# Kernel optimization log

Measured on AMD Instinct MI355X. Metric: run time of the kernel, lower is better.

Reference implementation:

```python
import jax, jax.numpy as jnp
import numpy as np

N = 50000      # nodes
E = 800000     # edges
IN = 128       # in_channels
HID = 32       # hidden_channels per head
HEADS = 4
OUT = 16       # out_channels
NEG_SLOPE_ATT = 0.2   # GATv2Conv default negative_slope
NEG_SLOPE_ACT = 0.01  # F.leaky_relu default
EPS = 1e-16


def setup_inputs() -> dict:
    key = jax.random.key(0)
    ks = jax.random.split(key, 13)
    d1 = HEADS * HID  # 128
    g = lambda k, shape, fan: jax.random.normal(k, shape, jnp.float32) * (1.0 / np.sqrt(fan))
    return {
        "x": jax.random.normal(ks[0], (N, IN), jnp.float32),
        "edge_index": jax.random.randint(ks[1], (2, E), 0, N, dtype=jnp.int32),
        "edge_weight": jax.random.uniform(ks[2], (E,), jnp.float32),
        # conv1 (GATv2): lin_l, lin_r, att, bias
        "Wl1": g(ks[3], (IN, d1), IN), "Wr1": g(ks[4], (IN, d1), IN),
        "att1": g(ks[5], (HEADS, HID), HID), "b1": jnp.zeros((d1,), jnp.float32),
        # conv2
        "Wl2": g(ks[6], (d1, d1), d1), "Wr2": g(ks[7], (d1, d1), d1),
        "att2": g(ks[8], (HEADS, HID), HID), "b2": jnp.zeros((d1,), jnp.float32),
        # classifier
        "Wc": g(ks[9], (d1, OUT), d1), "bc": jnp.zeros((OUT,), jnp.float32),
    }


def gatv2_layer(x, Wl, Wr, att, bias, src, dst):
    n = x.shape[0]
    xl = (x @ Wl).reshape(n, HEADS, HID)  # source transform
    xr = (x @ Wr).reshape(n, HEADS, HID)  # target transform
    m = xl[src] + xr[dst]                                    # [Etot, H, C]
    e = jnp.sum(jax.nn.leaky_relu(m, NEG_SLOPE_ATT) * att, axis=-1)  # [Etot, H]
    # segment softmax over incoming edges of each target node
    emax = jax.ops.segment_max(e, dst, num_segments=n)       # [N, H]
    ex = jnp.exp(e - emax[dst])
    denom = jax.ops.segment_sum(ex, dst, num_segments=n)     # [N, H]
    alpha = ex / (denom[dst] + EPS)                          # [Etot, H]
    out = jax.ops.segment_sum(xl[src] * alpha[:, :, None], dst, num_segments=n)  # [N, H, C]
    return out.reshape(n, HEADS * HID) + bias


def reference(x, edge_index, edge_weight, Wl1, Wr1, att1, b1, Wl2, Wr2, att2, b2, Wc, bc):
    # GATv2Conv default add_self_loops=True
    loops = jnp.arange(N, dtype=edge_index.dtype)
    src = jnp.concatenate([edge_index[0], loops])
    dst = jnp.concatenate([edge_index[1], loops])
    h = gatv2_layer(x, Wl1, Wr1, att1, b1, src, dst)
    h = jax.nn.leaky_relu(h, NEG_SLOPE_ACT)
    h = gatv2_layer(h, Wl2, Wr2, att2, b2, src, dst)
    h = jax.nn.leaky_relu(h, NEG_SLOPE_ACT)
    logits = h @ Wc + bc
    return (logits, h)
```

## Files before the change

### kernel.cpp

```cpp
#include <hip/hip_runtime.h>
#include <hip/hip_fp16.h>


#define LOG2E 1.4426950408889634f
#define AST 40

typedef short bf16x8 __attribute__((ext_vector_type(8)));
typedef float f32x4 __attribute__((ext_vector_type(4)));

__device__ __forceinline__ unsigned short f2bf(float f) {
  union { float f; unsigned u; } x; x.f = f;
  unsigned r = x.u + 0x7fffu + ((x.u >> 16) & 1u);
  return (unsigned short)(r >> 16);
}
__device__ __forceinline__ float bf2f(unsigned short h) {
  union { unsigned u; float f; } x; x.u = ((unsigned)h) << 16;
  return x.f;
}
__device__ __forceinline__ void split4(float4 v, ushort4& h, ushort4& l) {
  h.x = f2bf(v.x); l.x = f2bf(v.x - bf2f(h.x));
  h.y = f2bf(v.y); l.y = f2bf(v.y - bf2f(h.y));
  h.z = f2bf(v.z); l.z = f2bf(v.z - bf2f(h.z));
  h.w = f2bf(v.w); l.w = f2bf(v.w - bf2f(h.w));
}


__global__ __launch_bounds__(256) void zero_i32(int* __restrict__ p, int n) {
  int i = blockIdx.x * 256 + threadIdx.x;
  if (i < n) p[i] = 0;
}

__global__ __launch_bounds__(256) void count_kernel(const int* __restrict__ dst,
                                                    int* __restrict__ cnt, int E) {
  int i = blockIdx.x * 256 + threadIdx.x;
  if (i < E) atomicAdd(&cnt[dst[i]], 1);
}

__global__ __launch_bounds__(256) void scan_blk(const int* __restrict__ cnt,
                                                int* __restrict__ excl,
                                                int* __restrict__ bsum, int n) {
  __shared__ int s[256];
  int t = threadIdx.x, i = blockIdx.x * 256 + t;
  int v = (i < n) ? (cnt[i] + 1) : 0;
  s[t] = v;
  __syncthreads();
#pragma unroll
  for (int off = 1; off < 256; off <<= 1) {
    int u = (t >= off) ? s[t - off] : 0;
    __syncthreads();
    s[t] += u;
    __syncthreads();
  }
  if (i < n) excl[i] = s[t] - v;
  if (t == 255) bsum[blockIdx.x] = s[255];
}

__global__ __launch_bounds__(256) void scan_bsum(int* __restrict__ bsum, int nb,
                                                 int* __restrict__ row_start, int n) {
  __shared__ int s[256];
  int t = threadIdx.x;
  int v = (t < nb) ? bsum[t] : 0;
  s[t] = v;
  __syncthreads();
#pragma unroll
  for (int off = 1; off < 256; off <<= 1) {
    int u = (t >= off) ? s[t - off] : 0;
    __syncthreads();
    s[t] += u;
    __syncthreads();
  }
  if (t < nb) bsum[t] = s[t] - v;
  if (t == 255) row_start[n] = s[255];
}

__global__ __launch_bounds__(256) void scan_add(int* __restrict__ row_start,
                                                const int* __restrict__ bsum,
                                                int* __restrict__ wpos,
                                                int* __restrict__ csr,
                                                int n, int padBase) {
  int i = blockIdx.x * 256 + threadIdx.x;
  if (i < n) {
    int r = row_start[i] + bsum[blockIdx.x];
    row_start[i] = r;
    wpos[i] = r + 1;
    csr[r] = i;
  }
  if (blockIdx.x == 0 && threadIdx.x < 16) csr[padBase + threadIdx.x] = 0;
}

__global__ __launch_bounds__(256) void scatter_kernel(const int* __restrict__ src,
                                                      const int* __restrict__ dst,
                                                      int* __restrict__ wpos,
                                                      int* __restrict__ csr,
                                                      int E, int sliceSize) {
  int slice = blockIdx.x & 7;
  int chunk = blockIdx.x >> 3;
  int nchunk = gridDim.x >> 3;
  int lo = slice * sliceSize, hi = lo + sliceSize;
  int per = (E + nchunk - 1) / nchunk;
  int b = chunk * per;
  int e = min(b + per, E);
  for (int i = b + threadIdx.x; i < e; i += 256) {
    int d = dst[i];
    if (d >= lo && d < hi) {
      int p = atomicAdd(&wpos[d], 1);
      csr[p] = src[i];
    }
  }
}

__global__ __launch_bounds__(256) void convert_W(const float* __restrict__ Wl1,
                                                 const float* __restrict__ Wr1,
                                                 const float* __restrict__ Wl2,
                                                 const float* __restrict__ Wr2,
                                                 unsigned short* __restrict__ BT1h,
                                                 unsigned short* __restrict__ BT1l,
                                                 unsigned short* __restrict__ BT2h,
                                                 unsigned short* __restrict__ BT2l) {
  int b = blockIdx.x;
  const float* Wl = (b < 128) ? Wl1 : Wl2;
  const float* Wr = (b < 128) ? Wr1 : Wr2;
  unsigned short* BTh = (b < 128) ? BT1h : BT2h;
  unsigned short* BTl = (b < 128) ? BT1l : BT2l;
  int idx = (b & 127) * 256 + threadIdx.x;
  int col = idx >> 7, k = idx & 127;
  float v = (col < 128) ? Wl[k * 128 + col] : Wr[k * 128 + (col - 128)];
  unsigned short h = f2bf(v);
  BTh[idx] = h;
  BTl[idx] = f2bf(v - bf2f(h));
}

enum { IN_F32 = 0, IN_F16 = 1 };
template <int MODE>
__global__ __launch_bounds__(256) void gemm_mfma(
    const float* __restrict__ Af, const __half* __restrict__ Af16,
    const unsigned short* __restrict__ BTh, const unsigned short* __restrict__ BTl,
    __half* __restrict__ Cl, __half* __restrict__ Cr, int nrows) {
  __shared__ unsigned short sAh[128 * AST], sAl[128 * AST];
  __shared__ unsigned short sBh[128 * AST], sBl[128 * AST];
  int tid = threadIdx.x;
  int wave = tid >> 6, lane = tid & 63;
  int rowBase = blockIdx.x * 128;
  int colBase = blockIdx.y * 128;
  int rowHalf = (wave >> 1) * 64;
  int colHalf = (wave & 1) * 64;
  int l15 = lane & 15, quad = lane >> 4;

  f32x4 acc[4][4];
#pragma unroll
  for (int m = 0; m < 4; ++m)
#pragma unroll
    for (int n = 0; n < 4; ++n) acc[m][n] = (f32x4){0.f, 0.f, 0.f, 0.f};

  for (int kc = 0; kc < 4; ++kc) {
#pragma unroll
    for (int i = 0; i < 2; ++i) {
      int idx = tid + i * 256;
      int row = idx >> 2, seg = idx & 3;
      int gr = rowBase + row;
      if (MODE == IN_F32) {
        float4 v0 = make_float4(0.f, 0.f, 0.f, 0.f), v1 = v0;
        if (gr < nrows) {
          v0 = *(const float4*)&Af[(size_t)gr * 128 + kc * 32 + seg * 8];
          v1 = *(const float4*)&Af[(size_t)gr * 128 + kc * 32 + seg * 8 + 4];
        }
        ushort4 h0, l0, h1, l1;
        split4(v0, h0, l0);
        split4(v1, h1, l1);
        *(ushort4*)&sAh[row * AST + seg * 8] = h0;
        *(ushort4*)&sAh[row * AST + seg * 8 + 4] = h1;
        *(ushort4*)&sAl[row * AST + seg * 8] = l0;
        *(ushort4*)&sAl[row * AST + seg * 8 + 4] = l1;
      } else {
        uint4 raw = make_uint4(0, 0, 0, 0);
        if (gr < nrows)
          raw = *(const uint4*)&Af16[(size_t)gr * 128 + kc * 32 + seg * 8];
        const __half* hp = (const __half*)&raw;
        float4 v0 = make_float4(__half2float(hp[0]), __half2float(hp[1]),
                                __half2float(hp[2]), __half2float(hp[3]));
        float4 v1 = make_float4(__half2float(hp[4]), __half2float(hp[5]),
                                __half2float(hp[6]), __half2float(hp[7]));
        ushort4 h0, l0, h1, l1;
        split4(v0, h0, l0);
        split4(v1, h1, l1);
        *(ushort4*)&sAh[row * AST + seg * 8] = h0;
        *(ushort4*)&sAh[row * AST + seg * 8 + 4] = h1;
        *(ushort4*)&sAl[row * AST + seg * 8] = l0;
        *(ushort4*)&sAl[row * AST + seg * 8 + 4] = l1;
      }
    }
#pragma unroll
    for (int i = 0; i < 2; ++i) {
      int idx = tid + i * 256;
      int col = idx >> 2, seg = idx & 3;
      *(uint4*)&sBh[col * AST + seg * 8] =
          *(const uint4*)&BTh[(size_t)(colBase + col) * 128 + kc * 32 + seg * 8];
      *(uint4*)&sBl[col * AST + seg * 8] =
          *(const uint4*)&BTl[(size_t)(colBase + col) * 128 + kc * 32 + seg * 8];
    }
    __syncthreads();

    bf16x8 afh[4], afl[4], bfh[4], bfl[4];
#pragma unroll
    for (int m = 0; m < 4; ++m) {
      int r = rowHalf + m * 16 + l15;
      afh[m] = *(const bf16x8*)&sAh[r * AST + quad * 8];
      afl[m] = *(const bf16x8*)&sAl[r * AST + quad * 8];
    }
#pragma unroll
    for (int n = 0; n < 4; ++n) {
      int cc = colHalf + n * 16 + l15;
      bfh[n] = *(const bf16x8*)&sBh[cc * AST + quad * 8];
      bfl[n] = *(const bf16x8*)&sBl[cc * AST + quad * 8];
    }
#pragma unroll
    for (int m = 0; m < 4; ++m)
#pragma unroll
      for (int n = 0; n < 4; ++n) {
        acc[m][n] = __builtin_amdgcn_mfma_f32_16x16x32_bf16(afh[m], bfh[n], acc[m][n], 0, 0, 0);
        acc[m][n] = __builtin_amdgcn_mfma_f32_16x16x32_bf16(afh[m], bfl[n], acc[m][n], 0, 0, 0);
        acc[m][n] = __builtin_amdgcn_mfma_f32_16x16x32_bf16(afl[m], bfh[n], acc[m][n], 0, 0, 0);
      }
    __syncthreads();
  }

  __half* __restrict__ C = (blockIdx.y == 0) ? Cl : Cr;
#pragma unroll
  for (int m = 0; m < 4; ++m)
#pragma unroll
    for (int r = 0; r < 4; ++r) {
      int grow = rowBase + rowHalf + m * 16 + quad * 4 + r;
      if (grow < nrows) {
#pragma unroll
        for (int n = 0; n < 4; ++n)
          C[(size_t)grow * 128 + colHalf + n * 16 + l15] = __float2half(acc[m][n][r]);
      }
    }
}

__global__ __launch_bounds__(256) void gat_attn(const __half* __restrict__ xl,
                                                const __half* __restrict__ xr,
                                                const int* __restrict__ row_start,
                                                const int* __restrict__ csr,
                                                const float* __restrict__ att,
                                                const float* __restrict__ bias,
                                                float* __restrict__ ofp,
                                                __half* __restrict__ oh16,
                                                int n_nodes) {
  int node = blockIdx.x * 4 + (threadIdx.x >> 6);
  if (node >= n_nodes) return;
  int lane = threadIdx.x & 63;
  int slot = lane >> 4;
  int l15 = lane & 15;
  int c0 = l15 * 8;

  float fxr[8];
  {
    uint4 raw = *(const uint4*)&xr[(size_t)node * 128 + c0];
    const __half* hp = (const __half*)&raw;
#pragma unroll
    for (int k = 0; k < 8; ++k) fxr[k] = __half2float(hp[k]);
  }
  float a06[8], a04[8];
  {
    float4 a0 = *(const float4*)&att[c0];
    float4 a1 = *(const float4*)&att[c0 + 4];
    float av[8] = {a0.x, a0.y, a0.z, a0.w, a1.x, a1.y, a1.z, a1.w};
    const float C06 = 0.6f * LOG2E, C04 = 0.4f * LOG2E;
#pragma unroll
    for (int k = 0; k < 8; ++k) { a06[k] = av[k] * C06; a04[k] = av[k] * C04; }
  }

  float acc[8];
#pragma unroll
  for (int k = 0; k < 8; ++k) acc[k] = 0.f;
  float lsum = 0.f;

#define EDGE_BODY(SRC, PVALID)                                                 \
  {                                                                            \
    uint4 raw = *(const uint4*)&xl[(size_t)(unsigned)(SRC)*128 + c0];          \
    const __half* hp = (const __half*)&raw;                                    \
    float e = 0.f;                                                             \
    _Pragma("unroll") for (int k = 0; k < 8; ++k) {                            \
      float t = __half2float(hp[k]) + fxr[k];                                  \
      e = fmaf(a06[k], t, e);                                                  \
      e = fmaf(a04[k], fabsf(t), e);                                           \
    }                                                                          \
    e += __shfl_xor(e, 1);                                                     \
    e += __shfl_xor(e, 2);                                                     \
    float p = (PVALID) ? __builtin_amdgcn_exp2f(e) : 0.f;                      \
    lsum += p;                                                                 \
    _Pragma("unroll") for (int k = 0; k < 8; ++k)                              \
        acc[k] = fmaf(p, __half2float(hp[k]), acc[k]);                         \
  }

  int beg = row_start[node], end = row_start[node + 1];
  int deg = end - beg;
  int fullEnd = beg + (deg & ~15);

  for (int base = beg; base < fullEnd; base += 16) {
    int b0 = base + 4 * slot;
    int s0 = csr[b0], s1 = csr[b0 + 1], s2 = csr[b0 + 2], s3 = csr[b0 + 3];
    EDGE_BODY(s0, true);
    EDGE_BODY(s1, true);
    EDGE_BODY(s2, true);
    EDGE_BODY(s3, true);
  }
  for (int base = fullEnd; base < end; base += 4) {
    int idx = base + slot;
    int src = csr[idx];
    EDGE_BODY(src, idx < end);
  }
#undef EDGE_BODY

  lsum += __shfl_xor(lsum, 16);
  lsum += __shfl_xor(lsum, 32);
#pragma unroll
  for (int k = 0; k < 8; ++k) {
    acc[k] += __shfl_xor(acc[k], 16);
    acc[k] += __shfl_xor(acc[k], 32);
  }

  if (slot == 0) {
    float4 b0v = *(const float4*)&bias[c0];
    float4 b1v = *(const float4*)&bias[c0 + 4];
    float bv[8] = {b0v.x, b0v.y, b0v.z, b0v.w, b1v.x, b1v.y, b1v.z, b1v.w};
    float inv = 1.f / (lsum + 1e-16f);
    float o[8];
#pragma unroll
    for (int k = 0; k < 8; ++k) {
      float v = fmaf(acc[k], inv, bv[k]);
      o[k] = fmaf(0.495f, fabsf(v), 0.505f * v);
    }
    if (ofp) {
      *(float4*)&ofp[(size_t)node * 128 + c0] = make_float4(o[0], o[1], o[2], o[3]);
      *(float4*)&ofp[(size_t)node * 128 + c0 + 4] = make_float4(o[4], o[5], o[6], o[7]);
    }
    if (oh16) {
      ushort4 ha, hb;
      ha.x = __half_as_ushort(__float2half(o[0]));
      ha.y = __half_as_ushort(__float2half(o[1]));
      ha.z = __half_as_ushort(__float2half(o[2]));
      ha.w = __half_as_ushort(__float2half(o[3]));
      hb.x = __half_as_ushort(__float2half(o[4]));
      hb.y = __half_as_ushort(__float2half(o[5]));
      hb.z = __half_as_ushort(__float2half(o[6]));
      hb.w = __half_as_ushort(__float2half(o[7]));
      *(ushort4*)&oh16[(size_t)node * 128 + c0] = ha;
      *(ushort4*)&oh16[(size_t)node * 128 + c0 + 4] = hb;
    }
  }
}

__global__ __launch_bounds__(256) void classifier_kernel(const float4* __restrict__ h4,
                                                         const float* __restrict__ Wc,
                                                         const float* __restrict__ bc,
                                                         float* __restrict__ logits,
                                                         int n) {
  __shared__ float sW[2048];
  __shared__ float sb[16];
  int t = threadIdx.x;
#pragma unroll
  for (int i = 0; i < 8; ++i) sW[t + i * 256] = Wc[t + i * 256];
  if (t < 16) sb[t] = bc[t];
  __syncthreads();
  int node = blockIdx.x * 256 + t;
  if (node >= n) return;
  float acc[16];
#pragma unroll
  for (int o = 0; o < 16; ++o) acc[o] = sb[o];
  for (int c4 = 0; c4 < 32; ++c4) {
    float4 hv = h4[(unsigned)node * 32 + c4];
    const float* w = &sW[c4 * 64];
#pragma unroll
    for (int o = 0; o < 16; ++o) {
      acc[o] = fmaf(hv.x, w[o], acc[o]);
      acc[o] = fmaf(hv.y, w[16 + o], acc[o]);
      acc[o] = fmaf(hv.z, w[32 + o], acc[o]);
      acc[o] = fmaf(hv.w, w[48 + o], acc[o]);
    }
  }
#pragma unroll
  for (int q = 0; q < 4; ++q)
    *(float4*)&logits[(size_t)node * 16 + q * 4] =
        make_float4(acc[q * 4], acc[q * 4 + 1], acc[q * 4 + 2], acc[q * 4 + 3]);
}


extern "C" void kernel_launch(void* const* d_in, const int* in_sizes, int n_in,
                              void* d_out, int out_size, void* d_ws, size_t ws_size,
                              hipStream_t stream) {
  const float* x    = (const float*)d_in[0];
  const int*   ei   = (const int*)d_in[1];
  const float* Wl1  = (const float*)d_in[3];
  const float* Wr1  = (const float*)d_in[4];
  const float* att1 = (const float*)d_in[5];
  const float* b1   = (const float*)d_in[6];
  const float* Wl2  = (const float*)d_in[7];
  const float* Wr2  = (const float*)d_in[8];
  const float* att2 = (const float*)d_in[9];
  const float* b2   = (const float*)d_in[10];
  const float* Wc   = (const float*)d_in[11];
  const float* bc   = (const float*)d_in[12];

  const int N = in_sizes[0] / 128;
  const int E = in_sizes[1] / 2;

  float* outp   = (float*)d_out;
  float* logits = outp;
  float* hout   = outp + (size_t)N * 16;
  __half* h1f16 = (__half*)hout;

  char* ws = (char*)d_ws;
  __half* xlbuf = (__half*)ws;                ws += (size_t)N * 128 * 2;
  __half* xrbuf = (__half*)ws;                ws += (size_t)N * 128 * 2;
  unsigned short* WT1h = (unsigned short*)ws; ws += 256 * 128 * 2;
  unsigned short* WT1l = (unsigned short*)ws; ws += 256 * 128 * 2;
  unsigned short* WT2h = (unsigned short*)ws; ws += 256 * 128 * 2;
  unsigned short* WT2l = (unsigned short*)ws; ws += 256 * 128 * 2;
  int* cnt       = (int*)ws;                  ws += (size_t)N * 4;
  int* row_start = (int*)ws;                  ws += (size_t)(N + 1) * 4;
  int* wpos      = (int*)ws;                  ws += (size_t)N * 4;
  int* bsum      = (int*)ws;                  ws += 256 * 4;
  int* csr       = (int*)ws;                  ws += (size_t)(E + N + 16) * 4;

  const int* esrc = ei;
  const int* edst = ei + E;

  int gN = (N + 255) / 256, gE = (E + 255) / 256;
  dim3 gGemm((N + 127) / 128, 2);
  int gAttn = (N + 3) / 4;
  int sliceSize = (N + 7) / 8;

  zero_i32<<<gN, 256, 0, stream>>>(cnt, N);
  count_kernel<<<gE, 256, 0, stream>>>(edst, cnt, E);
  scan_blk<<<gN, 256, 0, stream>>>(cnt, row_start, bsum, N);
  scan_bsum<<<1, 256, 0, stream>>>(bsum, gN, row_start, N);
  scan_add<<<gN, 256, 0, stream>>>(row_start, bsum, wpos, csr, N, E + N);
  scatter_kernel<<<1024, 256, 0, stream>>>(esrc, edst, wpos, csr, E, sliceSize);

  convert_W<<<256, 256, 0, stream>>>(Wl1, Wr1, Wl2, Wr2, WT1h, WT1l, WT2h, WT2l);

  gemm_mfma<IN_F32><<<gGemm, 256, 0, stream>>>(x, nullptr, WT1h, WT1l,
                                               xlbuf, xrbuf, N);
  gat_attn<<<gAttn, 256, 0, stream>>>(xlbuf, xrbuf, row_start, csr, att1, b1,
                                      nullptr, h1f16, N);

  gemm_mfma<IN_F16><<<gGemm, 256, 0, stream>>>(nullptr, h1f16, WT2h, WT2l,
                                               xlbuf, xrbuf, N);
  gat_attn<<<gAttn, 256, 0, stream>>>(xlbuf, xrbuf, row_start, csr, att2, b2,
                                      hout, nullptr, N);

  classifier_kernel<<<(N + 255) / 256, 256, 0, stream>>>((const float4*)hout, Wc, bc,
                                                         logits, N);
}
```

Measured before the change: 323.3 us.

## Fuse CSR scatter into layer-1 GEMM, merge count with weight conversion, use packed fp16 math

```diff
diff --git a/kernel.cpp b/kernel.cpp
--- a/kernel.cpp
+++ b/kernel.cpp
@@ -24,16 +24,41 @@
   h.w = f2bf(v.w); l.w = f2bf(v.w - bf2f(h.w));
 }
 
+__device__ __forceinline__ float mixlo(float a, unsigned b, float c) {
+  float d;
+  asm("v_fma_mix_f32 %0, %1, %2, %3 op_sel_hi:[0,1,0]"
+      : "=v"(d) : "v"(a), "v"(b), "v"(c));
+  return d;
+}
+__device__ __forceinline__ float mixhi(float a, unsigned b, float c) {
+  float d;
+  asm("v_fma_mix_f32 %0, %1, %2, %3 op_sel:[0,1,0] op_sel_hi:[0,1,0]"
+      : "=v"(d) : "v"(a), "v"(b), "v"(c));
+  return d;
+}
+__device__ __forceinline__ float mixlo_abs(float a, unsigned b, float c) {
+  float d;
+  asm("v_fma_mix_f32 %0, %1, |%2|, %3 op_sel_hi:[0,1,0]"
+      : "=v"(d) : "v"(a), "v"(b), "v"(c));
+  return d;
+}
+__device__ __forceinline__ float mixhi_abs(float a, unsigned b, float c) {
+  float d;
+  asm("v_fma_mix_f32 %0, %1, |%2|, %3 op_sel:[0,1,0] op_sel_hi:[0,1,0]"
+      : "=v"(d) : "v"(a), "v"(b), "v"(c));
+  return d;
+}
+__device__ __forceinline__ unsigned pk_add(unsigned a, unsigned b) {
+  union { unsigned u; __half2 h; } x, y, r;
+  x.u = a; y.u = b;
+  r.h = __hadd2(x.h, y.h);
+  return r.u;
+}
+
 
 __global__ __launch_bounds__(256) void zero_i32(int* __restrict__ p, int n) {
   int i = blockIdx.x * 256 + threadIdx.x;
   if (i < n) p[i] = 0;
-}
-
-__global__ __launch_bounds__(256) void count_kernel(const int* __restrict__ dst,
-                                                    int* __restrict__ cnt, int E) {
-  int i = blockIdx.x * 256 + threadIdx.x;
-  if (i < E) atomicAdd(&cnt[dst[i]], 1);
 }
 
 __global__ __launch_bounds__(256) void scan_blk(const int* __restrict__ cnt,
@@ -88,36 +113,18 @@
   if (blockIdx.x == 0 && threadIdx.x < 16) csr[padBase + threadIdx.x] = 0;
 }
 
-__global__ __launch_bounds__(256) void scatter_kernel(const int* __restrict__ src,
-                                                      const int* __restrict__ dst,
-                                                      int* __restrict__ wpos,
-                                                      int* __restrict__ csr,
-                                                      int E, int sliceSize) {
-  int slice = blockIdx.x & 7;
-  int chunk = blockIdx.x >> 3;
-  int nchunk = gridDim.x >> 3;
-  int lo = slice * sliceSize, hi = lo + sliceSize;
-  int per = (E + nchunk - 1) / nchunk;
-  int b = chunk * per;
-  int e = min(b + per, E);
-  for (int i = b + threadIdx.x; i < e; i += 256) {
-    int d = dst[i];
-    if (d >= lo && d < hi) {
-      int p = atomicAdd(&wpos[d], 1);
-      csr[p] = src[i];
-    }
-  }
-}
-
-__global__ __launch_bounds__(256) void convert_W(const float* __restrict__ Wl1,
-                                                 const float* __restrict__ Wr1,
-                                                 const float* __restrict__ Wl2,
-                                                 const float* __restrict__ Wr2,
-                                                 unsigned short* __restrict__ BT1h,
-                                                 unsigned short* __restrict__ BT1l,
-                                                 unsigned short* __restrict__ BT2h,
-                                                 unsigned short* __restrict__ BT2l) {
+__global__ __launch_bounds__(256) void convert_count(
+    const float* __restrict__ Wl1, const float* __restrict__ Wr1,
+    const float* __restrict__ Wl2, const float* __restrict__ Wr2,
+    unsigned short* __restrict__ BT1h, unsigned short* __restrict__ BT1l,
+    unsigned short* __restrict__ BT2h, unsigned short* __restrict__ BT2l,
+    const int* __restrict__ dst, int* __restrict__ cnt, int E) {
   int b = blockIdx.x;
+  if (b >= 256) {
+    int i = (b - 256) * 256 + threadIdx.x;
+    if (i < E) atomicAdd(&cnt[dst[i]], 1);
+    return;
+  }
   const float* Wl = (b < 128) ? Wl1 : Wl2;
   const float* Wr = (b < 128) ? Wr1 : Wr2;
   unsigned short* BTh = (b < 128) ? BT1h : BT2h;
@@ -130,18 +137,66 @@
   BTl[idx] = f2bf(v - bf2f(h));
 }
 
-enum { IN_F32 = 0, IN_F16 = 1 };
-template <int MODE>
+enum { IN_F32 = 0, IN_BFPAIR = 1 };
+template <int MODE, int FUSE>
 __global__ __launch_bounds__(256) void gemm_mfma(
-    const float* __restrict__ Af, const __half* __restrict__ Af16,
+    const float* __restrict__ Af,
+    const unsigned short* __restrict__ Ah, const unsigned short* __restrict__ Al,
     const unsigned short* __restrict__ BTh, const unsigned short* __restrict__ BTl,
-    __half* __restrict__ Cl, __half* __restrict__ Cr, int nrows) {
-  __shared__ unsigned short sAh[128 * AST], sAl[128 * AST];
-  __shared__ unsigned short sBh[128 * AST], sBl[128 * AST];
+    __half* __restrict__ Cl, __half* __restrict__ Cr, int nrows,
+    const int* __restrict__ esrc, const int* __restrict__ edst,
+    int* __restrict__ wpos, int* __restrict__ csr, int E, int sliceSize) {
+  __shared__ __align__(16) unsigned short smem[4 * 128 * AST];
   int tid = threadIdx.x;
+  int bx, by;
+  if (FUSE) {
+    int g = blockIdx.x / 9, r = blockIdx.x - g * 9;
+    if (r < 5) {
+      int sid = g * 5 + r;
+      if (sid < 1024) {
+        int per = (E + 1023) >> 10;
+        int b0 = sid * per;
+        int cnt = min(per, E - b0);
+        if (cnt > 0) {
+          int* ss = (int*)smem;
+          int* sd = ss + per;
+          for (int i = tid; i < cnt; i += 256) {
+            ss[i] = esrc[b0 + i];
+            sd[i] = edst[b0 + i];
+          }
+          __syncthreads();
+          for (int sl = 0; sl < 8; ++sl) {
+            int lo = sl * sliceSize, hi = lo + sliceSize;
+            for (int i = tid; i < cnt; i += 256) {
+              int d = sd[i];
+              if (d >= lo && d < hi) {
+                int p = atomicAdd(&wpos[d], 1);
+                csr[p] = ss[i];
+              }
+            }
+          }
+        }
+      }
+      return;
+    }
+    int gid = g * 4 + (r - 5);
+    int nbx = (nrows + 127) >> 7;
+    if (gid >= nbx * 2) return;
+    bx = gid >> 1;
+    by = gid & 1;
+  } else {
+    bx = blockIdx.x;
+    by = blockIdx.y;
+  }
+
+  unsigned short* sAh = smem;
+  unsigned short* sAl = smem + 5120;
+  unsigned short* sBh = smem + 10240;
+  unsigned short* sBl = smem + 15360;
+
   int wave = tid >> 6, lane = tid & 63;
-  int rowBase = blockIdx.x * 128;
-  int colBase = blockIdx.y * 128;
+  int rowBase = bx * 128;
+  int colBase = by * 128;
   int rowHalf = (wave >> 1) * 64;
   int colHalf = (wave & 1) * 64;
   int l15 = lane & 15, quad = lane >> 4;
@@ -172,21 +227,13 @@
         *(ushort4*)&sAl[row * AST + seg * 8] = l0;
         *(ushort4*)&sAl[row * AST + seg * 8 + 4] = l1;
       } else {
-        uint4 raw = make_uint4(0, 0, 0, 0);
-        if (gr < nrows)
-          raw = *(const uint4*)&Af16[(size_t)gr * 128 + kc * 32 + seg * 8];
-        const __half* hp = (const __half*)&raw;
-        float4 v0 = make_float4(__half2float(hp[0]), __half2float(hp[1]),
-                                __half2float(hp[2]), __half2float(hp[3]));
-        float4 v1 = make_float4(__half2float(hp[4]), __half2float(hp[5]),
-                                __half2float(hp[6]), __half2float(hp[7]));
-        ushort4 h0, l0, h1, l1;
-        split4(v0, h0, l0);
-        split4(v1, h1, l1);
-        *(ushort4*)&sAh[row * AST + seg * 8] = h0;
-        *(ushort4*)&sAh[row * AST + seg * 8 + 4] = h1;
-        *(ushort4*)&sAl[row * AST + seg * 8] = l0;
-        *(ushort4*)&sAl[row * AST + seg * 8 + 4] = l1;
+        uint4 vh = make_uint4(0, 0, 0, 0), vl = vh;
+        if (gr < nrows) {
+          vh = *(const uint4*)&Ah[(size_t)gr * 128 + kc * 32 + seg * 8];
+          vl = *(const uint4*)&Al[(size_t)gr * 128 + kc * 32 + seg * 8];
+        }
+        *(uint4*)&sAh[row * AST + seg * 8] = vh;
+        *(uint4*)&sAl[row * AST + seg * 8] = vl;
       }
     }
 #pragma unroll
@@ -224,7 +271,7 @@
     __syncthreads();
   }
 
-  __half* __restrict__ C = (blockIdx.y == 0) ? Cl : Cr;
+  __half* __restrict__ C = (by == 0) ? Cl : Cr;
 #pragma unroll
   for (int m = 0; m < 4; ++m)
 #pragma unroll
@@ -245,7 +292,8 @@
                                                 const float* __restrict__ att,
                                                 const float* __restrict__ bias,
                                                 float* __restrict__ ofp,
-                                                __half* __restrict__ oh16,
+                                                unsigned short* __restrict__ ohi,
+                                                unsigned short* __restrict__ olo,
                                                 int n_nodes) {
   int node = blockIdx.x * 4 + (threadIdx.x >> 6);
   if (node >= n_nodes) return;
@@ -254,12 +302,11 @@
   int l15 = lane & 15;
   int c0 = l15 * 8;
 
-  float fxr[8];
+  unsigned hxr[4];
   {
     uint4 raw = *(const uint4*)&xr[(size_t)node * 128 + c0];
-    const __half* hp = (const __half*)&raw;
-#pragma unroll
-    for (int k = 0; k < 8; ++k) fxr[k] = __half2float(hp[k]);
+    const unsigned* q = (const unsigned*)&raw;
+    hxr[0] = q[0]; hxr[1] = q[1]; hxr[2] = q[2]; hxr[3] = q[3];
   }
   float a06[8], a04[8];
   {
@@ -279,19 +326,24 @@
 #define EDGE_BODY(SRC, PVALID)                                                 \
   {                                                                            \
     uint4 raw = *(const uint4*)&xl[(size_t)(unsigned)(SRC)*128 + c0];          \
-    const __half* hp = (const __half*)&raw;                                    \
-    float e = 0.f;                                                             \
-    _Pragma("unroll") for (int k = 0; k < 8; ++k) {                            \
-      float t = __half2float(hp[k]) + fxr[k];                                  \
-      e = fmaf(a06[k], t, e);                                                  \
-      e = fmaf(a04[k], fabsf(t), e);                                           \
+    const unsigned* xp = (const unsigned*)&raw;                                \
+    float e0 = 0.f, e1 = 0.f;                                                  \
+    _Pragma("unroll") for (int j = 0; j < 4; ++j) {                            \
+      unsigned tw = pk_add(xp[j], hxr[j]);                                     \
+      e0 = mixlo(a06[2 * j], tw, e0);                                          \
+      e0 = mixlo_abs(a04[2 * j], tw, e0);                                      \
+      e1 = mixhi(a06[2 * j + 1], tw, e1);                                      \
+      e1 = mixhi_abs(a04[2 * j + 1], tw, e1);                                  \
     }                                                                          \
+    float e = e0 + e1;                                                         \
     e += __shfl_xor(e, 1);                                                     \
     e += __shfl_xor(e, 2);                                                     \
     float p = (PVALID) ? __builtin_amdgcn_exp2f(e) : 0.f;                      \
     lsum += p;                                                                 \
-    _Pragma("unroll") for (int k = 0; k < 8; ++k)                              \
-        acc[k] = fmaf(p, __half2float(hp[k]), acc[k]);                         \
+    _Pragma("unroll") for (int j = 0; j < 4; ++j) {                            \
+      acc[2 * j] = mixlo(p, xp[j], acc[2 * j]);                                \
+      acc[2 * j + 1] = mixhi(p, xp[j], acc[2 * j + 1]);                        \
+    }                                                                          \
   }
 
   int beg = row_start[node], end = row_start[node + 1];
@@ -336,18 +388,20 @@
       *(float4*)&ofp[(size_t)node * 128 + c0] = make_float4(o[0], o[1], o[2], o[3]);
       *(float4*)&ofp[(size_t)node * 128 + c0 + 4] = make_float4(o[4], o[5], o[6], o[7]);
     }
-    if (oh16) {
-      ushort4 ha, hb;
-      ha.x = __half_as_ushort(__float2half(o[0]));
-      ha.y = __half_as_ushort(__float2half(o[1]));
-      ha.z = __half_as_ushort(__float2half(o[2]));
-      ha.w = __half_as_ushort(__float2half(o[3]));
-      hb.x = __half_as_ushort(__float2half(o[4]));
-      hb.y = __half_as_ushort(__float2half(o[5]));
-      hb.z = __half_as_ushort(__float2half(o[6]));
-      hb.w = __half_as_ushort(__float2half(o[7]));
-      *(ushort4*)&oh16[(size_t)node * 128 + c0] = ha;
-      *(ushort4*)&oh16[(size_t)node * 128 + c0 + 4] = hb;
+    if (ohi) {
+      ushort4 h0, h1, lo0, lo1;
+      h0.x = f2bf(o[0]); lo0.x = f2bf(o[0] - bf2f(h0.x));
+      h0.y = f2bf(o[1]); lo0.y = f2bf(o[1] - bf2f(h0.y));
+      h0.z = f2bf(o[2]); lo0.z = f2bf(o[2] - bf2f(h0.z));
+      h0.w = f2bf(o[3]); lo0.w = f2bf(o[3] - bf2f(h0.w));
+      h1.x = f2bf(o[4]); lo1.x = f2bf(o[4] - bf2f(h1.x));
+      h1.y = f2bf(o[5]); lo1.y = f2bf(o[5] - bf2f(h1.y));
+      h1.z = f2bf(o[6]); lo1.z = f2bf(o[6] - bf2f(h1.z));
+      h1.w = f2bf(o[7]); lo1.w = f2bf(o[7] - bf2f(h1.w));
+      *(ushort4*)&ohi[(size_t)node * 128 + c0] = h0;
+      *(ushort4*)&ohi[(size_t)node * 128 + c0 + 4] = h1;
+      *(ushort4*)&olo[(size_t)node * 128 + c0] = lo0;
+      *(ushort4*)&olo[(size_t)node * 128 + c0 + 4] = lo1;
     }
   }
 }
@@ -409,7 +463,8 @@
   float* outp   = (float*)d_out;
   float* logits = outp;
   float* hout   = outp + (size_t)N * 16;
-  __half* h1f16 = (__half*)hout;
+  unsigned short* h1h = (unsigned short*)hout;
+  unsigned short* h1l = h1h + (size_t)N * 128;
 
   char* ws = (char*)d_ws;
   __half* xlbuf = (__half*)ws;                ws += (size_t)N * 128 * 2;
@@ -428,28 +483,35 @@
   const int* edst = ei + E;
 
   int gN = (N + 255) / 256, gE = (E + 255) / 256;
-  dim3 gGemm((N + 127) / 128, 2);
   int gAttn = (N + 3) / 4;
   int sliceSize = (N + 7) / 8;
 
+  int nbx = (N + 127) / 128;
+  int nGemm = nbx * 2;
+  int groups = (1024 + 4) / 5;
+  int g2 = (nGemm + 3) / 4;
+  if (g2 > groups) groups = g2;
+  int gFused = groups * 9;
+
   zero_i32<<<gN, 256, 0, stream>>>(cnt, N);
-  count_kernel<<<gE, 256, 0, stream>>>(edst, cnt, E);
+  convert_count<<<256 + gE, 256, 0, stream>>>(Wl1, Wr1, Wl2, Wr2,
+                                              WT1h, WT1l, WT2h, WT2l,
+                                              edst, cnt, E);
   scan_blk<<<gN, 256, 0, stream>>>(cnt, row_start, bsum, N);
   scan_bsum<<<1, 256, 0, stream>>>(bsum, gN, row_start, N);
   scan_add<<<gN, 256, 0, stream>>>(row_start, bsum, wpos, csr, N, E + N);
-  scatter_kernel<<<1024, 256, 0, stream>>>(esrc, edst, wpos, csr, E, sliceSize);
-
-  convert_W<<<256, 256, 0, stream>>>(Wl1, Wr1, Wl2, Wr2, WT1h, WT1l, WT2h, WT2l);
-
-  gemm_mfma<IN_F32><<<gGemm, 256, 0, stream>>>(x, nullptr, WT1h, WT1l,
-                                               xlbuf, xrbuf, N);
+
+  gemm_mfma<IN_F32, 1><<<gFused, 256, 0, stream>>>(
+      x, nullptr, nullptr, WT1h, WT1l, xlbuf, xrbuf, N,
+      esrc, edst, wpos, csr, E, sliceSize);
   gat_attn<<<gAttn, 256, 0, stream>>>(xlbuf, xrbuf, row_start, csr, att1, b1,
-                                      nullptr, h1f16, N);
-
-  gemm_mfma<IN_F16><<<gGemm, 256, 0, stream>>>(nullptr, h1f16, WT2h, WT2l,
-                                               xlbuf, xrbuf, N);
+                                      nullptr, h1h, h1l, N);
+
+  gemm_mfma<IN_BFPAIR, 0><<<dim3(nbx, 2), 256, 0, stream>>>(
+      nullptr, h1h, h1l, WT2h, WT2l, xlbuf, xrbuf, N,
+      nullptr, nullptr, nullptr, nullptr, 0, 0);
   gat_attn<<<gAttn, 256, 0, stream>>>(xlbuf, xrbuf, row_start, csr, att2, b2,
-                                      hout, nullptr, N);
+                                      hout, nullptr, nullptr, N);
 
   classifier_kernel<<<(N + 255) / 256, 256, 0, stream>>>((const float4*)hout, Wc, bc,
                                                          logits, N);
```

Result: no change. 319.4 us (-1.2%).
